# Optimization experiments

Measured on AMD Instinct MI355X. Metric: run time of the kernel, lower is better.

The kernel has to match this reference:

```python
import jax, jax.numpy as jnp
import numpy as np

B, S, E, H = 8, 2048, 512, 8
HD = E // H
N_IND = 64


def setup_inputs() -> dict:
    key = jax.random.key(0)
    ks = jax.random.split(key, 10)
    s = 1.0 / np.sqrt(E)
    return {
        "x": jax.random.normal(ks[0], (B, S, E), jnp.float32),
        "Wq": jax.random.normal(ks[1], (E, E), jnp.float32) * s,
        "bq": jax.random.normal(ks[2], (E,), jnp.float32) * s,
        "Wk": jax.random.normal(ks[3], (E, E), jnp.float32) * s,
        "bk": jax.random.normal(ks[4], (E,), jnp.float32) * s,
        "Wv": jax.random.normal(ks[5], (E, E), jnp.float32) * s,
        "bv": jax.random.normal(ks[6], (E,), jnp.float32) * s,
        "Wo": jax.random.normal(ks[7], (E, E), jnp.float32) * s,
        "bo": jax.random.normal(ks[8], (E,), jnp.float32) * s,
        "industry_ids": jax.random.randint(ks[9], (S,), 0, N_IND, jnp.int32),
    }


def reference(x, Wq, bq, Wk, bk, Wv, bv, Wo, bo, industry_ids):
    # same-industry block mask [S, S]; every row attends at least to itself
    mask = industry_ids[:, None] == industry_ids[None, :]
    # projections (torch Linear: y = x @ W.T + b)
    q = (x @ Wq.T + bq).reshape(B, S, H, HD).transpose(0, 2, 1, 3)  # [B,H,S,HD]
    k = (x @ Wk.T + bk).reshape(B, S, H, HD).transpose(0, 2, 1, 3)
    v = (x @ Wv.T + bv).reshape(B, S, H, HD).transpose(0, 2, 1, 3)
    scores = jnp.einsum("bhqd,bhkd->bhqk", q, k) / np.sqrt(HD).astype(jnp.float32)
    scores = jnp.where(mask[None, None, :, :], scores, -jnp.inf)
    attn = jax.nn.softmax(scores, axis=-1)  # dropout is identity at inference
    out = jnp.einsum("bhqk,bhkd->bhqd", attn, v)
    out = out.transpose(0, 2, 1, 3).reshape(B, S, E)
    return out @ Wo.T + bo
```

## Files before the change

kernel.cpp:

```cpp
#include <hip/hip_runtime.h>
#include <cstdint>

#define DEVFN __device__ __forceinline__

typedef __bf16 bf16x8 __attribute__((ext_vector_type(8)));
typedef float f32x4 __attribute__((ext_vector_type(4)));
typedef unsigned int uint;

constexpr int Bc = 8, Sc = 2048, Ec = 512, Hc = 8, HDc = 64, NI = 64;
constexpr int Mtot = Bc * Sc;
constexpr int Kdim = Ec;
constexpr int MAXITEMS = 128;

DEVFN unsigned short f2bf(float f) {
  unsigned u = __builtin_bit_cast(unsigned, f);
  u += 0x7fffu + ((u >> 16) & 1u);
  return (unsigned short)(u >> 16);
}

typedef const void __attribute__((address_space(1))) gvoid_t;
typedef void __attribute__((address_space(3))) lvoid_t;
DEVFN void gload16(const void* g, void* l) {
  __builtin_amdgcn_global_load_lds((gvoid_t*)g, (lvoid_t*)l, 16, 0, 0);
}

DEVFN uint cvtpk(float lo, float hi) {
  uint r;
  asm("v_cvt_pk_bf16_f32 %0, %1, %2" : "=v"(r) : "v"(lo), "v"(hi));
  return r;
}

__global__ void cvt_x_kernel(const float* __restrict__ x, const int* __restrict__ perm,
                             ushort* __restrict__ xb) {
  int i = blockIdx.x * 256 + threadIdx.x;
  int mp = i >> 7;
  int c = i & 127;
  int b = mp >> 11, p = mp & (Sc - 1);
  int srow = (b << 11) | perm[p];
  float4 v = *(const float4*)(x + (size_t)srow * Ec + c * 4);
  ushort4 o = {f2bf(v.x), f2bf(v.y), f2bf(v.z), f2bf(v.w)};
  ((ushort4*)xb)[i] = o;
}

__global__ void cvt_w_kernel(const float* __restrict__ Wq, const float* __restrict__ Wk,
                             const float* __restrict__ Wv, const float* __restrict__ Wo,
                             ushort* __restrict__ Wcat, ushort* __restrict__ Wob) {
  int i = blockIdx.x * 256 + threadIdx.x;
  int idx = i * 4;
  int n = idx >> 9, k = idx & 511;
  const float* src;
  ushort* dst;
  if (n < 512)       { src = Wq + (size_t)n * 512 + k;          dst = Wcat + (size_t)n * 512 + k; }
  else if (n < 1024) { src = Wk + (size_t)(n - 512) * 512 + k;  dst = Wcat + (size_t)n * 512 + k; }
  else if (n < 1536) { src = Wv + (size_t)(n - 1024) * 512 + k; dst = Wcat + (size_t)n * 512 + k; }
  else               { src = Wo + (size_t)(n - 1536) * 512 + k; dst = Wob + (size_t)(n - 1536) * 512 + k; }
  float4 v = *(const float4*)src;
  ushort4 o = {f2bf(v.x), f2bf(v.y), f2bf(v.z), f2bf(v.w)};
  *(ushort4*)dst = o;
}

__global__ void sort_kernel(const int* __restrict__ ids, int* __restrict__ perm,
                            int* __restrict__ gstart, int* __restrict__ gsz,
                            int* __restrict__ items, int* __restrict__ nitems) {
  __shared__ int sid[Sc];
  __shared__ int hist[NI];
  __shared__ int base[NI];
  int t = threadIdx.x;
  if (t < NI) hist[t] = 0;
  for (int i = t; i < Sc; i += 256) sid[i] = ids[i];
  __syncthreads();
  for (int i = t; i < Sc; i += 256) atomicAdd(&hist[sid[i]], 1);
  __syncthreads();
  if (t == 0) {
    int run = 0;
    for (int g = 0; g < NI; ++g) { base[g] = run; run += hist[g]; }
    int cnt = 0;
    for (int g = 0; g < NI; ++g)
      for (int q0 = 0; q0 < hist[g]; q0 += 32) items[cnt++] = (g << 16) | q0;
    *nitems = cnt;
  }
  __syncthreads();
  if (t < NI) { gstart[t] = base[t]; gsz[t] = hist[t]; }
  int lane = t & 63, w = t >> 6;
  for (int g = w; g < NI; g += 4) {
    int run = base[g];
    for (int c = 0; c < Sc; c += 64) {
      int tok = c + lane;
      int id = sid[tok];
      unsigned long long mask = __ballot(id == g);
      if (id == g) {
        int rank = __popcll(mask & ((1ull << lane) - 1ull));
        perm[run + rank] = tok;
      }
      run += __popcll(mask);
    }
  }
}

template <int NTOT, bool QKV>
__global__ __launch_bounds__(256) void gemm_bt(
    const ushort* __restrict__ A, const ushort* __restrict__ Bw,
    const float* __restrict__ bias0, const float* __restrict__ bias1,
    const float* __restrict__ bias2, const int* __restrict__ permarg,
    ushort* __restrict__ qkvout, float* __restrict__ out) {
  constexpr int NK = Kdim / 64;
  __shared__ __align__(16) char ldsraw[65536];
  ushort* sAb = (ushort*)ldsraw;
  ushort* sBb = (ushort*)(ldsraw + 32768);
  const int tid = threadIdx.x;
  const int lane = tid & 63;
  const int wave = tid >> 6;
  const int wr = wave >> 1, wc = wave & 1;
  const int orig = blockIdx.x;
  const int xcd = orig & 7, gl = orig >> 3;
  const int mbase = (xcd * 16 + (gl & 15)) * 128;
  const int nbase = (gl >> 4) * 128;

  f32x4 acc[4][4] = {};

  const int rowS = wave * 32 + (lane >> 3);
  const int kc = lane & 7;

  auto stage = [&](int buf, int kt) {
    const int k0 = kt * 64;
#pragma unroll
    for (int c = 0; c < 4; ++c) {
      int row = rowS + c * 8;
      int kcp = (kc ^ (row & 7)) * 8;
      gload16(A + (size_t)(mbase + row) * Kdim + k0 + kcp,
              sAb + buf * 8192 + (wave * 256 + c * 64) * 8);
      gload16(Bw + (size_t)(nbase + row) * Kdim + k0 + kcp,
              sBb + buf * 8192 + (wave * 256 + c * 64) * 8);
    }
  };

  stage(0, 0);
  stage(1, 1);

  for (int kt = 0; kt < NK; ++kt) {
    const int cur = kt & 1;
    if (kt < NK - 1) {
      asm volatile("s_waitcnt vmcnt(8)" ::: "memory");
    } else {
      asm volatile("s_waitcnt vmcnt(0)" ::: "memory");
    }
    __builtin_amdgcn_sched_barrier(0);
    __builtin_amdgcn_s_barrier();
    __builtin_amdgcn_sched_barrier(0);

    const char* Ab = (const char*)(sAb + cur * 8192);
    const char* Bb = (const char*)(sBb + cur * 8192);
    __builtin_amdgcn_s_setprio(1);
#pragma unroll
    for (int kk = 0; kk < 2; ++kk) {
      bf16x8 af[4], bfv[4];
#pragma unroll
      for (int i = 0; i < 4; ++i) {
        int row = wr * 64 + i * 16 + (lane & 15);
        int off = row * 128 + kk * 64 + (lane >> 4) * 16;
        off ^= (row & 7) << 4;
        af[i] = *(const bf16x8*)(Ab + off);
      }
#pragma unroll
      for (int j = 0; j < 4; ++j) {
        int col = wc * 64 + j * 16 + (lane & 15);
        int off = col * 128 + kk * 64 + (lane >> 4) * 16;
        off ^= (col & 7) << 4;
        bfv[j] = *(const bf16x8*)(Bb + off);
      }
#pragma unroll
      for (int i = 0; i < 4; ++i)
#pragma unroll
        for (int j = 0; j < 4; ++j)
          acc[i][j] = __builtin_amdgcn_mfma_f32_16x16x32_bf16(af[i], bfv[j], acc[i][j], 0, 0, 0);
    }
    __builtin_amdgcn_s_setprio(0);

    asm volatile("s_waitcnt lgkmcnt(0)" ::: "memory");
    __builtin_amdgcn_sched_barrier(0);
    __builtin_amdgcn_s_barrier();
    __builtin_amdgcn_sched_barrier(0);
    if (kt + 2 < NK) stage(cur, kt + 2);
  }

  if constexpr (QKV) {
    ushort* T = (ushort*)ldsraw;
#pragma unroll
    for (int i = 0; i < 4; ++i) {
#pragma unroll
      for (int j = 0; j < 4; ++j) {
        int nl = wc * 64 + j * 16 + (lane & 15);
        int n = nbase + nl;
        float bv = (n < 512) ? bias0[n] : (n < 1024) ? bias1[n - 512] : bias2[n - 1024];
#pragma unroll
        for (int r = 0; r < 4; ++r) {
          int ml = wr * 64 + i * 16 + (lane >> 4) * 4 + r;
          T[ml * 136 + nl] = f2bf(acc[i][j][r] + bv);
        }
      }
    }
    __syncthreads();
#pragma unroll
    for (int k = 0; k < 8; ++k) {
      int c = tid + 256 * k;
      int row = c >> 4, col8 = (c & 15) * 8;
      uint4 w = *(const uint4*)(T + row * 136 + col8);
      int n0 = nbase + col8;
      int proj = n0 >> 9, h = (n0 >> 6) & 7, d0 = n0 & 63;
      int p = mbase + row;
      int bidx = p >> 11, pl = p & (Sc - 1);
      size_t off = (size_t)proj * ((size_t)Bc * Hc * Sc * HDc) +
                   (size_t)((bidx * Hc + h) * Sc + pl) * HDc + d0;
      *(uint4*)(qkvout + off) = w;
    }
  } else {
    float* T = (float*)ldsraw;
#pragma unroll
    for (int i = 0; i < 4; ++i) {
#pragma unroll
      for (int j = 0; j < 4; ++j) {
        int nl = wc * 64 + j * 16 + (lane & 15);
        float bv = bias0[nbase + nl];
#pragma unroll
        for (int r = 0; r < 4; ++r) {
          int ml = wr * 64 + i * 16 + (lane >> 4) * 4 + r;
          T[ml * 128 + nl] = acc[i][j][r] + bv;
        }
      }
    }
    __syncthreads();
#pragma unroll
    for (int k = 0; k < 16; ++k) {
      int c = tid + 256 * k;
      int row = c >> 5, col4 = (c & 31) * 4;
      float4 w = *(const float4*)(T + row * 128 + col4);
      int p = mbase + row;
      int bidx = p >> 11;
      int orow = (bidx << 11) | permarg[p & (Sc - 1)];
      *(float4*)(out + (size_t)orow * NTOT + nbase + col4) = w;
    }
  }
}

__global__ __launch_bounds__(64) void attn5_kernel(
    const ushort* __restrict__ qkv, const int* __restrict__ gstart,
    const int* __restrict__ gsz, const int* __restrict__ items,
    const int* __restrict__ nitems, ushort* __restrict__ obuf) {
  __shared__ __align__(16) ushort vt[64 * 40];
  if ((int)blockIdx.x >= *nitems) return;
  const int iv = items[blockIdx.x];
  const int g = iv >> 16, q0 = iv & 0xffff;
  const int bh = blockIdx.y;
  const int start = gstart[g], n = gsz[g];
  const int lane = threadIdx.x;
  const int ql = lane & 15, lg = lane >> 4;

  const size_t planeSz = (size_t)Bc * Hc * Sc * HDc;
  const ushort* qb = qkv + (size_t)bh * Sc * HDc;
  const ushort* kb = qb + planeSz;
  const ushort* vb = kb + planeSz;

  bf16x8 qf[2][2];
#pragma unroll
  for (int qt = 0; qt < 2; ++qt) {
    int row = min(start + q0 + qt * 16 + ql, Sc - 1);
#pragma unroll
    for (int h = 0; h < 2; ++h)
      qf[qt][h] = *(const bf16x8*)(qb + (size_t)row * HDc + h * 32 + lg * 8);
  }

  f32x4 oacc[2][4] = {};
  float lsum[2] = {0.f, 0.f};

  const int vk = lane & 31;
  const int vh = (lane >> 5) * 32;
  const int Lbase = 4 * (ql + 32 * (lg & 1));

  const int npair = (n + 31) >> 5;
  for (int pr = 0; pr < npair; ++pr) {
    const int c0 = pr * 32;
    int vrow = min(start + c0 + vk, Sc - 1);
    const uint4* vp = (const uint4*)(vb + (size_t)vrow * HDc + vh);
    uint4 v0 = vp[0], v1 = vp[1], v2 = vp[2], v3 = vp[3];

    bf16x8 kf[2][2];
#pragma unroll
    for (int t = 0; t < 2; ++t) {
      int row = min(start + c0 + t * 16 + ql, Sc - 1);
#pragma unroll
      for (int h = 0; h < 2; ++h)
        kf[t][h] = *(const bf16x8*)(kb + (size_t)row * HDc + h * 32 + lg * 8);
    }

    uint pw[2][4];
#pragma unroll
    for (int qt = 0; qt < 2; ++qt) {
      f32x4 s0 = {}, s1 = {};
      s0 = __builtin_amdgcn_mfma_f32_16x16x32_bf16(kf[0][0], qf[qt][0], s0, 0, 0, 0);
      s0 = __builtin_amdgcn_mfma_f32_16x16x32_bf16(kf[0][1], qf[qt][1], s0, 0, 0, 0);
      s1 = __builtin_amdgcn_mfma_f32_16x16x32_bf16(kf[1][0], qf[qt][0], s1, 0, 0, 0);
      s1 = __builtin_amdgcn_mfma_f32_16x16x32_bf16(kf[1][1], qf[qt][1], s1, 0, 0, 0);
      float p0[4], p1[4];
      float ls = 0.f;
#pragma unroll
      for (int r = 0; r < 4; ++r) {
        int kk = c0 + 4 * lg + r;
        float e0 = (kk < n) ? __expf(s0[r] * 0.125f) : 0.f;
        float e1 = (kk + 16 < n) ? __expf(s1[r] * 0.125f) : 0.f;
        p0[r] = e0;
        p1[r] = e1;
        ls += e0 + e1;
      }
      lsum[qt] += ls;
      uint a0 = cvtpk(p0[0], p0[1]), b0 = cvtpk(p0[2], p0[3]);
      uint a1 = cvtpk(p1[0], p1[1]), b1 = cvtpk(p1[2], p1[3]);
      uint pA0 = __builtin_amdgcn_ds_bpermute(Lbase, a0);
      uint pB0 = __builtin_amdgcn_ds_bpermute(Lbase, b0);
      uint pA1 = __builtin_amdgcn_ds_bpermute(Lbase, a1);
      uint pB1 = __builtin_amdgcn_ds_bpermute(Lbase, b1);
      uint pC0 = __builtin_amdgcn_ds_bpermute(Lbase + 64, a0);
      uint pD0 = __builtin_amdgcn_ds_bpermute(Lbase + 64, b0);
      uint pC1 = __builtin_amdgcn_ds_bpermute(Lbase + 64, a1);
      uint pD1 = __builtin_amdgcn_ds_bpermute(Lbase + 64, b1);
      bool t0 = lg < 2;
      pw[qt][0] = t0 ? pA0 : pA1;
      pw[qt][1] = t0 ? pB0 : pB1;
      pw[qt][2] = t0 ? pC0 : pC1;
      pw[qt][3] = t0 ? pD0 : pD1;
    }

    {
      uint w[16] = {v0.x, v0.y, v0.z, v0.w, v1.x, v1.y, v1.z, v1.w,
                    v2.x, v2.y, v2.z, v2.w, v3.x, v3.y, v3.z, v3.w};
#pragma unroll
      for (int i = 0; i < 16; ++i) {
        vt[(vh + 2 * i) * 40 + vk] = (ushort)(w[i] & 0xffffu);
        vt[(vh + 2 * i + 1) * 40 + vk] = (ushort)(w[i] >> 16);
      }
    }
    asm volatile("s_waitcnt lgkmcnt(0)" ::: "memory");
    __builtin_amdgcn_sched_barrier(0);
    bf16x8 vf[4];
#pragma unroll
    for (int dq = 0; dq < 4; ++dq)
      vf[dq] = *(const bf16x8*)(vt + (dq * 16 + ql) * 40 + lg * 8);
    asm volatile("s_waitcnt lgkmcnt(0)" ::: "memory");
    __builtin_amdgcn_sched_barrier(0);
#pragma unroll
    for (int qt = 0; qt < 2; ++qt) {
      union { uint u[4]; bf16x8 v; } pf;
      pf.u[0] = pw[qt][0]; pf.u[1] = pw[qt][1]; pf.u[2] = pw[qt][2]; pf.u[3] = pw[qt][3];
#pragma unroll
      for (int dq = 0; dq < 4; ++dq)
        oacc[qt][dq] = __builtin_amdgcn_mfma_f32_16x16x32_bf16(vf[dq], pf.v, oacc[qt][dq], 0, 0, 0);
    }
  }

#pragma unroll
  for (int qt = 0; qt < 2; ++qt) {
    float l = lsum[qt];
    l += __shfl_xor(l, 16);
    l += __shfl_xor(l, 32);
    float inv = 1.f / l;
    int qi = q0 + qt * 16 + ql;
    if (qi < n) {
      int p = start + qi;
      ushort* op = obuf + (size_t)((bh >> 3) * Sc + p) * Ec + (bh & 7) * HDc + lg * 4;
#pragma unroll
      for (int dq = 0; dq < 4; ++dq) {
        uint w0 = cvtpk(oacc[qt][dq][0] * inv, oacc[qt][dq][1] * inv);
        uint w1 = cvtpk(oacc[qt][dq][2] * inv, oacc[qt][dq][3] * inv);
        uint2 wv = {w0, w1};
        *(uint2*)(op + dq * 16) = wv;
      }
    }
  }
}

extern "C" void kernel_launch(void* const* d_in, const int* in_sizes, int n_in,
                              void* d_out, int out_size, void* d_ws, size_t ws_size,
                              hipStream_t stream) {
  const float* x  = (const float*)d_in[0];
  const float* Wq = (const float*)d_in[1];
  const float* bq = (const float*)d_in[2];
  const float* Wk = (const float*)d_in[3];
  const float* bk = (const float*)d_in[4];
  const float* Wv = (const float*)d_in[5];
  const float* bv = (const float*)d_in[6];
  const float* Wo = (const float*)d_in[7];
  const float* bo = (const float*)d_in[8];
  const int* ids  = (const int*)d_in[9];
  float* out = (float*)d_out;

  char* ws = (char*)d_ws;
  ushort* xb   = (ushort*)(ws);
  ushort* Wcat = (ushort*)(ws + 16777216);
  ushort* Wob  = (ushort*)(ws + 18350080);
  ushort* qkv  = (ushort*)(ws + 18874368);
  ushort* obuf = (ushort*)(ws + 69206016);
  int* perm    = (int*)(ws + 85983232);
  int* gstart  = perm + Sc;
  int* gsz     = gstart + NI;
  int* items   = gsz + NI;
  int* nitems  = items + MAXITEMS;

  sort_kernel<<<dim3(1), dim3(256), 0, stream>>>(ids, perm, gstart, gsz, items, nitems);
  cvt_x_kernel<<<dim3(Mtot * Ec / 4 / 256), dim3(256), 0, stream>>>(x, perm, xb);
  cvt_w_kernel<<<dim3(2048 * 512 / 4 / 256), dim3(256), 0, stream>>>(Wq, Wk, Wv, Wo, Wcat, Wob);
  gemm_bt<1536, true><<<dim3(Mtot / 128 * 12), dim3(256), 0, stream>>>(
      xb, Wcat, bq, bk, bv, perm, qkv, (float*)nullptr);
  attn5_kernel<<<dim3(MAXITEMS, Bc * Hc), dim3(64), 0, stream>>>(qkv, gstart, gsz, items,
                                                                 nitems, obuf);
  gemm_bt<512, false><<<dim3(Mtot / 128 * 4), dim3(256), 0, stream>>>(
      obuf, Wob, bo, bo, bo, perm, (ushort*)nullptr, out);
}
```

Before: 128.5 us.

## Use 256x256 tiles with 512 threads for the QKV projection GEMM

The QKV projection GEMM moves from 128x128 tiles with 4 waves to 256x256 tiles with 8 waves and 128KB of LDS. Each wave now computes a 128x64 sub-tile, which doubles the reuse of every staged A and B slice and cuts global and LDS traffic per FLOP. The grid shrinks from 1536 to 384 blocks, which hurts wave balance across CUs, and the larger accumulators (32 f32x4 per wave) raise register pressure. The waitcnt-plus-barrier sequences are also merged into single inline-asm macros, and the output GEMM is split into its own non-templated kernel.

New measurement: 134.5 us. 1.05x slower.

```diff
diff --git a/kernel.cpp b/kernel.cpp
--- a/kernel.cpp
+++ b/kernel.cpp
@@ -29,6 +29,17 @@
   asm("v_cvt_pk_bf16_f32 %0, %1, %2" : "=v"(r) : "v"(lo), "v"(hi));
   return r;
 }
+
+#define WAIT_VM_BARRIER(N)                                            \
+  do {                                                                \
+    asm volatile("s_waitcnt vmcnt(" #N ")\n\ts_barrier" ::: "memory"); \
+    __builtin_amdgcn_sched_barrier(0);                                \
+  } while (0)
+#define WAIT_LGKM_BARRIER()                                            \
+  do {                                                                 \
+    asm volatile("s_waitcnt lgkmcnt(0)\n\ts_barrier" ::: "memory");    \
+    __builtin_amdgcn_sched_barrier(0);                                 \
+  } while (0)
 
 __global__ void cvt_x_kernel(const float* __restrict__ x, const int* __restrict__ perm,
                              ushort* __restrict__ xb) {
@@ -97,13 +108,124 @@
   }
 }
 
-template <int NTOT, bool QKV>
-__global__ __launch_bounds__(256) void gemm_bt(
+__global__ __launch_bounds__(512) void gemm_qkv256(
     const ushort* __restrict__ A, const ushort* __restrict__ Bw,
     const float* __restrict__ bias0, const float* __restrict__ bias1,
-    const float* __restrict__ bias2, const int* __restrict__ permarg,
-    ushort* __restrict__ qkvout, float* __restrict__ out) {
+    const float* __restrict__ bias2, ushort* __restrict__ qkvout) {
   constexpr int NK = Kdim / 64;
+  __shared__ __align__(16) char ldsraw[131072];
+  ushort* sAb = (ushort*)ldsraw;
+  ushort* sBb = (ushort*)(ldsraw + 65536);
+  const int tid = threadIdx.x;
+  const int lane = tid & 63;
+  const int wave = tid >> 6;
+  const int wm = wave >> 2;
+  const int wn = wave & 3;
+  const int orig = blockIdx.x;
+  const int xcd = orig & 7, gl = orig >> 3;
+  const int mbase = (xcd * 8 + (gl & 7)) * 256;
+  const int nbase = (gl >> 3) * 256;
+
+  f32x4 acc[8][4] = {};
+
+  const int rowS = tid >> 3;
+  const int kc = tid & 7;
+
+  auto stage = [&](int buf, int kt) {
+    const int k0 = kt * 64;
+#pragma unroll
+    for (int c = 0; c < 4; ++c) {
+      int row = rowS + c * 64;
+      int kcp = (kc ^ (row & 7)) * 8;
+      gload16(A + (size_t)(mbase + row) * Kdim + k0 + kcp,
+              sAb + buf * 16384 + (wave * 64 + c * 512) * 8);
+      gload16(Bw + (size_t)(nbase + row) * Kdim + k0 + kcp,
+              sBb + buf * 16384 + (wave * 64 + c * 512) * 8);
+    }
+  };
+
+  stage(0, 0);
+  stage(1, 1);
+
+  for (int kt = 0; kt < NK; ++kt) {
+    const int cur = kt & 1;
+    if (kt < NK - 1) {
+      WAIT_VM_BARRIER(8);
+    } else {
+      WAIT_VM_BARRIER(0);
+    }
+
+    const char* Ab = (const char*)(sAb + cur * 16384);
+    const char* Bb = (const char*)(sBb + cur * 16384);
+    __builtin_amdgcn_s_setprio(1);
+#pragma unroll
+    for (int kk = 0; kk < 2; ++kk) {
+      bf16x8 af[8], bfv[4];
+#pragma unroll
+      for (int i = 0; i < 8; ++i) {
+        int row = wm * 128 + i * 16 + (lane & 15);
+        int off = row * 128 + kk * 64 + (lane >> 4) * 16;
+        off ^= (row & 7) << 4;
+        af[i] = *(const bf16x8*)(Ab + off);
+      }
+#pragma unroll
+      for (int j = 0; j < 4; ++j) {
+        int col = wn * 64 + j * 16 + (lane & 15);
+        int off = col * 128 + kk * 64 + (lane >> 4) * 16;
+        off ^= (col & 7) << 4;
+        bfv[j] = *(const bf16x8*)(Bb + off);
+      }
+#pragma unroll
+      for (int i = 0; i < 8; ++i)
+#pragma unroll
+        for (int j = 0; j < 4; ++j)
+          acc[i][j] = __builtin_amdgcn_mfma_f32_16x16x32_bf16(af[i], bfv[j], acc[i][j], 0, 0, 0);
+    }
+    __builtin_amdgcn_s_setprio(0);
+
+    WAIT_LGKM_BARRIER();
+    if (kt + 2 < NK) stage(cur, kt + 2);
+  }
+
+  {
+    ushort* T = (ushort*)ldsraw;
+#pragma unroll
+    for (int i = 0; i < 8; ++i) {
+#pragma unroll
+      for (int j = 0; j < 4; ++j) {
+        int nl = wn * 64 + j * 16 + (lane & 15);
+        int n = nbase + nl;
+        float bv = (n < 512) ? bias0[n] : (n < 1024) ? bias1[n - 512] : bias2[n - 1024];
+#pragma unroll
+        for (int r = 0; r < 4; ++r) {
+          int ml = wm * 128 + i * 16 + (lane >> 4) * 4 + r;
+          T[ml * 256 + nl] = f2bf(acc[i][j][r] + bv);
+        }
+      }
+    }
+    __syncthreads();
+#pragma unroll
+    for (int k = 0; k < 16; ++k) {
+      int c = tid + 512 * k;
+      int row = c >> 5, col8 = (c & 31) * 8;
+      uint4 w = *(const uint4*)(T + row * 256 + col8);
+      int n0 = nbase + col8;
+      int proj = n0 >> 9, h = (n0 >> 6) & 7, d0 = n0 & 63;
+      int p = mbase + row;
+      int bidx = p >> 11, pl = p & (Sc - 1);
+      size_t off = (size_t)proj * ((size_t)Bc * Hc * Sc * HDc) +
+                   (size_t)((bidx * Hc + h) * Sc + pl) * HDc + d0;
+      *(uint4*)(qkvout + off) = w;
+    }
+  }
+}
+
+__global__ __launch_bounds__(256) void gemm_out128(
+    const ushort* __restrict__ A, const ushort* __restrict__ Bw,
+    const float* __restrict__ bias0, const int* __restrict__ permarg,
+    float* __restrict__ out) {
+  constexpr int NK = Kdim / 64;
+  constexpr int NTOT = 512;
   __shared__ __align__(16) char ldsraw[65536];
   ushort* sAb = (ushort*)ldsraw;
   ushort* sBb = (ushort*)(ldsraw + 32768);
@@ -140,13 +262,10 @@
   for (int kt = 0; kt < NK; ++kt) {
     const int cur = kt & 1;
     if (kt < NK - 1) {
-      asm volatile("s_waitcnt vmcnt(8)" ::: "memory");
+      WAIT_VM_BARRIER(8);
     } else {
-      asm volatile("s_waitcnt vmcnt(0)" ::: "memory");
-    }
-    __builtin_amdgcn_sched_barrier(0);
-    __builtin_amdgcn_s_barrier();
-    __builtin_amdgcn_sched_barrier(0);
+      WAIT_VM_BARRIER(0);
+    }
 
     const char* Ab = (const char*)(sAb + cur * 8192);
     const char* Bb = (const char*)(sBb + cur * 8192);
@@ -176,69 +295,34 @@
     }
     __builtin_amdgcn_s_setprio(0);
 
-    asm volatile("s_waitcnt lgkmcnt(0)" ::: "memory");
-    __builtin_amdgcn_sched_barrier(0);
-    __builtin_amdgcn_s_barrier();
-    __builtin_amdgcn_sched_barrier(0);
+    WAIT_LGKM_BARRIER();
     if (kt + 2 < NK) stage(cur, kt + 2);
   }
 
-  if constexpr (QKV) {
-    ushort* T = (ushort*)ldsraw;
-#pragma unroll
-    for (int i = 0; i < 4; ++i) {
-#pragma unroll
-      for (int j = 0; j < 4; ++j) {
-        int nl = wc * 64 + j * 16 + (lane & 15);
-        int n = nbase + nl;
-        float bv = (n < 512) ? bias0[n] : (n < 1024) ? bias1[n - 512] : bias2[n - 1024];
-#pragma unroll
-        for (int r = 0; r < 4; ++r) {
-          int ml = wr * 64 + i * 16 + (lane >> 4) * 4 + r;
-          T[ml * 136 + nl] = f2bf(acc[i][j][r] + bv);
-        }
-      }
-    }
-    __syncthreads();
-#pragma unroll
-    for (int k = 0; k < 8; ++k) {
-      int c = tid + 256 * k;
-      int row = c >> 4, col8 = (c & 15) * 8;
-      uint4 w = *(const uint4*)(T + row * 136 + col8);
-      int n0 = nbase + col8;
-      int proj = n0 >> 9, h = (n0 >> 6) & 7, d0 = n0 & 63;
-      int p = mbase + row;
-      int bidx = p >> 11, pl = p & (Sc - 1);
-      size_t off = (size_t)proj * ((size_t)Bc * Hc * Sc * HDc) +
-                   (size_t)((bidx * Hc + h) * Sc + pl) * HDc + d0;
-      *(uint4*)(qkvout + off) = w;
-    }
-  } else {
-    float* T = (float*)ldsraw;
-#pragma unroll
-    for (int i = 0; i < 4; ++i) {
-#pragma unroll
-      for (int j = 0; j < 4; ++j) {
-        int nl = wc * 64 + j * 16 + (lane & 15);
-        float bv = bias0[nbase + nl];
-#pragma unroll
-        for (int r = 0; r < 4; ++r) {
-          int ml = wr * 64 + i * 16 + (lane >> 4) * 4 + r;
-          T[ml * 128 + nl] = acc[i][j][r] + bv;
-        }
-      }
-    }
-    __syncthreads();
-#pragma unroll
-    for (int k = 0; k < 16; ++k) {
-      int c = tid + 256 * k;
-      int row = c >> 5, col4 = (c & 31) * 4;
-      float4 w = *(const float4*)(T + row * 128 + col4);
-      int p = mbase + row;
-      int bidx = p >> 11;
-      int orow = (bidx << 11) | permarg[p & (Sc - 1)];
-      *(float4*)(out + (size_t)orow * NTOT + nbase + col4) = w;
-    }
+  float* T = (float*)ldsraw;
+#pragma unroll
+  for (int i = 0; i < 4; ++i) {
+#pragma unroll
+    for (int j = 0; j < 4; ++j) {
+      int nl = wc * 64 + j * 16 + (lane & 15);
+      float bv = bias0[nbase + nl];
+#pragma unroll
+      for (int r = 0; r < 4; ++r) {
+        int ml = wr * 64 + i * 16 + (lane >> 4) * 4 + r;
+        T[ml * 128 + nl] = acc[i][j][r] + bv;
+      }
+    }
+  }
+  __syncthreads();
+#pragma unroll
+  for (int k = 0; k < 16; ++k) {
+    int c = tid + 256 * k;
+    int row = c >> 5, col4 = (c & 31) * 4;
+    float4 w = *(const float4*)(T + row * 128 + col4);
+    int p = mbase + row;
+    int bidx = p >> 11;
+    int orow = (bidx << 11) | permarg[p & (Sc - 1)];
+    *(float4*)(out + (size_t)orow * NTOT + nbase + col4) = w;
   }
 }
 
@@ -407,10 +491,8 @@
   sort_kernel<<<dim3(1), dim3(256), 0, stream>>>(ids, perm, gstart, gsz, items, nitems);
   cvt_x_kernel<<<dim3(Mtot * Ec / 4 / 256), dim3(256), 0, stream>>>(x, perm, xb);
   cvt_w_kernel<<<dim3(2048 * 512 / 4 / 256), dim3(256), 0, stream>>>(Wq, Wk, Wv, Wo, Wcat, Wob);
-  gemm_bt<1536, true><<<dim3(Mtot / 128 * 12), dim3(256), 0, stream>>>(
-      xb, Wcat, bq, bk, bv, perm, qkv, (float*)nullptr);
+  gemm_qkv256<<<dim3(Mtot / 256 * 6), dim3(512), 0, stream>>>(xb, Wcat, bq, bk, bv, qkv);
   attn5_kernel<<<dim3(MAXITEMS, Bc * Hc), dim3(64), 0, stream>>>(qkv, gstart, gsz, items,
                                                                  nitems, obuf);
-  gemm_bt<512, false><<<dim3(Mtot / 128 * 4), dim3(256), 0, stream>>>(
-      obuf, Wob, bo, bo, bo, perm, (ushort*)nullptr, out);
-}
+  gemm_out128<<<dim3(Mtot / 128 * 4), dim3(256), 0, stream>>>(obuf, Wob, bo, perm, out);
+}
```
